# Optimization experiments

Hardware: AMD Instinct MI355X
Metric: run time of the kernel (lower is better)

The kernel has to match this reference:

```python
import jax, jax.numpy as jnp
import numpy as np

HIDDEN = 1280
NUM_HEADS = 16
NUM_KV_HEADS = 4
HEAD_DIM = 80
Q_SIZE = NUM_HEADS * HEAD_DIM          # 1280
KV_SIZE = NUM_KV_HEADS * HEAD_DIM      # 320
QKV_OUT = Q_SIZE + 2 * KV_SIZE         # 1920
R_SOFTPLUS_0 = 1.442695041


def setup_inputs() -> dict:
    key = jax.random.key(0)
    ks = jax.random.split(key, 6)
    B, S = 4, 2048
    return {
        "hidden_states": jax.random.normal(ks[0], (B, S, HIDDEN), dtype=jnp.float32),
        "scaling": jax.random.normal(ks[1], (HEAD_DIM,), dtype=jnp.float32),
        "qkv_w": jax.random.normal(ks[2], (QKV_OUT, HIDDEN), dtype=jnp.float32) * (1.0 / np.sqrt(HIDDEN)),
        "qkv_b": jax.random.normal(ks[3], (QKV_OUT,), dtype=jnp.float32) * 0.01,
        "o_w": jax.random.normal(ks[4], (HIDDEN, Q_SIZE), dtype=jnp.float32) * (1.0 / np.sqrt(Q_SIZE)),
        "o_b": jax.random.normal(ks[5], (HIDDEN,), dtype=jnp.float32) * 0.01,
    }


def reference(hidden_states, scaling, qkv_w, qkv_b, o_w, o_b):
    B, S, _ = hidden_states.shape
    qkv = hidden_states @ qkv_w.T + qkv_b                      # [B,S,1920]
    xq = qkv[..., :Q_SIZE].reshape(B, S, NUM_HEADS, HEAD_DIM)
    xk = qkv[..., Q_SIZE:Q_SIZE + KV_SIZE].reshape(B, S, NUM_KV_HEADS, HEAD_DIM)
    xv = qkv[..., Q_SIZE + KV_SIZE:].reshape(B, S, NUM_KV_HEADS, HEAD_DIM)
    # learned per-head-dim scaling: (r_softplus_0/sqrt(d)) * softplus(scaling)
    scale = (R_SOFTPLUS_0 / np.sqrt(HEAD_DIM)) * jax.nn.softplus(scaling)
    xq = xq * scale[None, None, None, :]
    # GQA: expand kv heads to match query heads (repeat_interleave on head dim)
    nq_per_kv = NUM_HEADS // NUM_KV_HEADS
    k = jnp.repeat(xk, nq_per_kv, axis=2)                      # [B,S,H,d]
    v = jnp.repeat(xv, nq_per_kv, axis=2)
    scores = jnp.einsum("bqhd,bkhd->bhqk", xq, k)              # [B,H,S,S]
    probs = jax.nn.softmax(scores.astype(jnp.float32), axis=-1).astype(xq.dtype)
    out = jnp.einsum("bhqk,bkhd->bqhd", probs, v)              # [B,S,H,d]
    out = out.reshape(B, S, Q_SIZE)
    return out @ o_w.T + o_b
```

## Files before the change

kernel.cpp:

```cpp
#include <hip/hip_runtime.h>

#define HIDDEN 1280
#define QOUT   1920
#define QSIZE  1280
#define KVSIZE 320
#define NHEAD  16
#define NKV    4
#define DH     80
#define SEQ    2048
#define BATCH  4
#define MTOT   (BATCH * SEQ)
#define NT64   (SEQ / 64)
#define KTILE_ELEMS 6144
#define VTILE_ELEMS 5760

typedef __attribute__((ext_vector_type(8))) short bf16x8;
typedef __attribute__((ext_vector_type(4))) float f32x4;

__device__ __forceinline__ unsigned short f2bf(float x) {
  union { float f; unsigned u; } v; v.f = x;
  unsigned r = v.u + 0x7fffu + ((v.u >> 16) & 1u);
  return (unsigned short)(r >> 16);
}

__device__ __forceinline__ unsigned packbf(float a, float b) {
  union { float f; unsigned u; } ua, ub;
  ua.f = a; ub.f = b;
  return __builtin_amdgcn_perm(ub.u + 0x8000u, ua.u + 0x8000u, 0x07060302u);
}

__device__ __forceinline__ float exp2x(float x) {
#if __has_builtin(__builtin_amdgcn_exp2f)
  return __builtin_amdgcn_exp2f(x);
#else
  return exp2f(x);
#endif
}

__device__ __forceinline__ void async_copy16(const void* g, void* lds) {
  __builtin_amdgcn_global_load_lds(
      (const __attribute__((address_space(1))) unsigned int*)g,
      (__attribute__((address_space(3))) unsigned int*)lds, 16, 0, 0);
}

#define HSB   (MTOT * HIDDEN / 4 / 256)
#define QWB   (QOUT * HIDDEN / 4 / 256)
#define OWB   (HIDDEN * QSIZE / 4 / 256)
__global__ __launch_bounds__(256) void prep_k(const float* __restrict__ hs,
                                              const float* __restrict__ qkv_w,
                                              const float* __restrict__ o_w,
                                              const float* __restrict__ scaling,
                                              unsigned short* __restrict__ hs_bf,
                                              unsigned short* __restrict__ qkvw_bf,
                                              unsigned short* __restrict__ ow_bf,
                                              float* __restrict__ cs) {
  const int bid = blockIdx.x, tid = threadIdx.x;
  const float* src; unsigned short* dst; int i;
  if (bid < HSB)            { src = hs;    dst = hs_bf;   i = bid * 256 + tid; }
  else if (bid < HSB + QWB) { src = qkv_w; dst = qkvw_bf; i = (bid - HSB) * 256 + tid; }
  else if (bid < HSB + QWB + OWB) { src = o_w; dst = ow_bf; i = (bid - HSB - QWB) * 256 + tid; }
  else {
    int n = (bid - HSB - QWB - OWB) * 256 + tid;
    if (n < QOUT) {
      float v = 1.0f;
      if (n < QSIZE) {
        float x = scaling[n % DH];
        float sp = (x > 20.f) ? x : log1pf(__expf(x));
        v = 1.442695041f * 1.442695041f * 0.11180339887f * sp;
      }
      cs[n] = v;
    }
    return;
  }
  float4 v = ((const float4*)src)[i];
  ushort4 o;
  o.x = f2bf(v.x); o.y = f2bf(v.y); o.z = f2bf(v.z); o.w = f2bf(v.w);
  ((ushort4*)dst)[i] = o;
}

template <bool OUT_BF16, bool USE_SCALE>
__global__ __launch_bounds__(256) void gemm_bt(const unsigned short* __restrict__ A,
                                               const unsigned short* __restrict__ Bt,
                                               const float* __restrict__ bias,
                                               const float* __restrict__ colscale,
                                               void* __restrict__ Cout,
                                               int M, int N, int K) {
  __shared__ unsigned short As[128 * 64];
  __shared__ unsigned short Bs[128 * 64];
  const int tid  = threadIdx.x;
  const int wave = tid >> 6, lane = tid & 63;
  const int r = lane & 15, quad = lane >> 4;
  const int xm = r & 7;
  const int m0 = blockIdx.y * 128, n0 = blockIdx.x * 128;
  const int rm = (wave >> 1) * 64, cn = (wave & 1) * 64;

  f32x4 acc[4][4];
#pragma unroll
  for (int i = 0; i < 4; ++i)
#pragma unroll
    for (int j = 0; j < 4; ++j) acc[i][j] = f32x4{0.f, 0.f, 0.f, 0.f};

  for (int k0 = 0; k0 < K; k0 += 64) {
    __syncthreads();
#pragma unroll
    for (int j = 0; j < 4; ++j) {
      const int c = tid + j * 256;
      const int row = c >> 3, sp = c & 7;
      const int sd = (sp ^ (row & 7)) * 8;
      async_copy16(A  + (size_t)(m0 + row) * K + k0 + sd, &As[c * 8]);
      async_copy16(Bt + (size_t)(n0 + row) * K + k0 + sd, &Bs[c * 8]);
    }
    __syncthreads();
#pragma unroll
    for (int kk = 0; kk < 2; ++kk) {
      bf16x8 af[4], bfr[4];
#pragma unroll
      for (int mi = 0; mi < 4; ++mi)
        af[mi] = *(const bf16x8*)&As[(rm + mi * 16 + r) * 64 + ((kk * 4 + quad) ^ xm) * 8];
#pragma unroll
      for (int ni = 0; ni < 4; ++ni)
        bfr[ni] = *(const bf16x8*)&Bs[(cn + ni * 16 + r) * 64 + ((kk * 4 + quad) ^ xm) * 8];
#pragma unroll
      for (int mi = 0; mi < 4; ++mi)
#pragma unroll
        for (int ni = 0; ni < 4; ++ni)
          acc[mi][ni] = __builtin_amdgcn_mfma_f32_16x16x32_bf16(af[mi], bfr[ni], acc[mi][ni], 0, 0, 0);
    }
  }

#pragma unroll
  for (int ni = 0; ni < 4; ++ni) {
    const int n = n0 + cn + ni * 16 + r;
    const float bn = bias[n];
    const float sc = USE_SCALE ? colscale[n] : 1.0f;
#pragma unroll
    for (int mi = 0; mi < 4; ++mi) {
#pragma unroll
      for (int reg = 0; reg < 4; ++reg) {
        const int m = m0 + rm + mi * 16 + quad * 4 + reg;
        const float v = (acc[mi][ni][reg] + bn) * sc;
        if (OUT_BF16)
          ((unsigned short*)Cout)[(size_t)m * N + n] = f2bf(v);
        else
          ((float*)Cout)[(size_t)m * N + n] = v;
      }
    }
  }
}

__global__ __launch_bounds__(256) void kvpack(const unsigned short* __restrict__ qkv,
                                              unsigned short* __restrict__ Kp,
                                              unsigned short* __restrict__ Vp) {
  const int st = blockIdx.x, kvh = blockIdx.y, b = blockIdx.z;
  const int tid = threadIdx.x;
  unsigned short* kout = Kp + (size_t)((b * NKV + kvh) * NT64 + st) * KTILE_ELEMS;
#pragma unroll
  for (int j = 0; j < 3; ++j) {
    int c = tid + j * 256;
    int row = c / 12, cir = c - row * 12;
    int kk = cir >> 2, sp = cir & 3;
    int sd = sp ^ ((row >> 1) & 3);
    int d0 = kk * 32 + sd * 8;
    uint4 v = {0, 0, 0, 0};
    if (d0 < DH)
      v = *(const uint4*)&qkv[(size_t)(b * SEQ + st * 64 + row) * QOUT +
                              QSIZE + kvh * DH + d0];
    *(uint4*)&kout[row * 96 + kk * 32 + sp * 8] = v;
  }
  __shared__ unsigned short tile[64][88];
  for (int c = tid; c < 640; c += 256) {
    int row = c / 10, seg = c % 10;
    uint4 v = *(const uint4*)&qkv[(size_t)(b * SEQ + st * 64 + row) * QOUT +
                                  QSIZE + KVSIZE + kvh * DH + seg * 8];
    *(uint4*)&tile[row][seg * 8] = v;
  }
  __syncthreads();
  unsigned short* vout = Vp + (size_t)((b * NKV + kvh) * NT64 + st) * VTILE_ELEMS;
  for (int c = tid; c < 5120; c += 256) {
    int d = c >> 6, key = c & 63;
    vout[d * 72 + key] = tile[key][d];
  }
}

__global__ __launch_bounds__(256, 2) void attn(const unsigned short* __restrict__ qkv,
                                               const unsigned short* __restrict__ Kp,
                                               const unsigned short* __restrict__ Vp,
                                               unsigned short* __restrict__ att) {
  const int qt = blockIdx.x, h = blockIdx.y, b = blockIdx.z;
  const int kvh = h >> 2;
  const int tid = threadIdx.x;
  const int wave = tid >> 6, lane = tid & 63;
  const int r = lane & 15, quad = lane >> 4;
  const int sq8 = (quad ^ ((r >> 1) & 3)) * 8;

  __shared__ unsigned short Ks[64 * 96];
  __shared__ unsigned short Vs[96 * 72];
  __shared__ unsigned short Ps[4][64 * 72];

  {
    const uint4 ones = {0x3F803F80u, 0x3F803F80u, 0x3F803F80u, 0x3F803F80u};
    for (int c = tid; c < 144; c += 256)
      *(uint4*)&Vs[80 * 72 + c * 8] = ones;
  }

  const int qbase = qt * 256 + wave * 64;
  bf16x8 qb[4][3];
#pragma unroll
  for (int t = 0; t < 4; ++t)
#pragma unroll
    for (int kk = 0; kk < 3; ++kk)
      qb[t][kk] = *(const bf16x8*)&qkv[(size_t)(b * SEQ + qbase + t * 16 + r) * QOUT +
                                       h * DH + kk * 32 + quad * 8];

  f32x4 o_acc[6][4];
#pragma unroll
  for (int i = 0; i < 6; ++i)
#pragma unroll
    for (int t = 0; t < 4; ++t) o_acc[i][t] = f32x4{0.f, 0.f, 0.f, 0.f};

  const unsigned short* kp = Kp + (size_t)((b * NKV + kvh) * NT64) * KTILE_ELEMS;
  const unsigned short* vp = Vp + (size_t)((b * NKV + kvh) * NT64) * VTILE_ELEMS;

  for (int kt = 0; kt < NT64; ++kt) {
    __syncthreads();
#pragma unroll
    for (int j = 0; j < 3; ++j)
      async_copy16(kp + (size_t)kt * KTILE_ELEMS + (tid + j * 256) * 8,
                   &Ks[(tid + j * 256) * 8]);
#pragma unroll
    for (int j = 0; j < 3; ++j) {
      int c = tid + j * 256;
      if (c < 720)
        async_copy16(vp + (size_t)kt * VTILE_ELEMS + c * 8, &Vs[c * 8]);
    }
    __syncthreads();

    f32x4 s[4][4];
#pragma unroll
    for (int nt = 0; nt < 4; ++nt) {
#pragma unroll
      for (int t = 0; t < 4; ++t) s[nt][t] = f32x4{0.f, 0.f, 0.f, 0.f};
#pragma unroll
      for (int kk = 0; kk < 3; ++kk) {
        bf16x8 ka = *(const bf16x8*)&Ks[(nt * 16 + r) * 96 + kk * 32 + sq8];
#pragma unroll
        for (int t = 0; t < 4; ++t)
          s[nt][t] = __builtin_amdgcn_mfma_f32_16x16x32_bf16(ka, qb[t][kk], s[nt][t], 0, 0, 0);
      }
    }

#pragma unroll
    for (int t = 0; t < 4; ++t)
#pragma unroll
      for (int nt = 0; nt < 4; ++nt) {
        uint2 w;
        w.x = packbf(exp2x(s[nt][t][0]), exp2x(s[nt][t][1]));
        w.y = packbf(exp2x(s[nt][t][2]), exp2x(s[nt][t][3]));
        *(uint2*)&Ps[wave][(t * 16 + r) * 72 + nt * 16 + quad * 4] = w;
      }
    __asm__ volatile("s_waitcnt lgkmcnt(0)" ::: "memory");

#pragma unroll
    for (int kh = 0; kh < 2; ++kh) {
      bf16x8 pb[4];
#pragma unroll
      for (int t = 0; t < 4; ++t)
        pb[t] = *(const bf16x8*)&Ps[wave][(t * 16 + r) * 72 + kh * 32 + quad * 8];
#pragma unroll
      for (int nt2 = 0; nt2 < 6; ++nt2) {
        bf16x8 va = *(const bf16x8*)&Vs[(nt2 * 16 + r) * 72 + kh * 32 + quad * 8];
#pragma unroll
        for (int t = 0; t < 4; ++t)
          o_acc[nt2][t] = __builtin_amdgcn_mfma_f32_16x16x32_bf16(va, pb[t], o_acc[nt2][t], 0, 0, 0);
      }
    }
  }

#pragma unroll
  for (int t = 0; t < 4; ++t) {
    const float il = 1.0f / o_acc[5][t][0];
    const size_t q = (size_t)(b * SEQ + qbase + t * 16 + r);
#pragma unroll
    for (int nt2 = 0; nt2 < 5; ++nt2) {
      uint2 w;
      w.x = packbf(o_acc[nt2][t][0] * il, o_acc[nt2][t][1] * il);
      w.y = packbf(o_acc[nt2][t][2] * il, o_acc[nt2][t][3] * il);
      *(uint2*)&att[q * QSIZE + h * DH + nt2 * 16 + quad * 4] = w;
    }
  }
}

extern "C" void kernel_launch(void* const* d_in, const int* in_sizes, int n_in,
                              void* d_out, int out_size, void* d_ws, size_t ws_size,
                              hipStream_t stream) {
  const float* hs      = (const float*)d_in[0];
  const float* scaling = (const float*)d_in[1];
  const float* qkv_w   = (const float*)d_in[2];
  const float* qkv_b   = (const float*)d_in[3];
  const float* o_w     = (const float*)d_in[4];
  const float* o_b     = (const float*)d_in[5];

  char* p = (char*)d_ws;
  unsigned short* hs_bf   = (unsigned short*)p; p += (size_t)MTOT * HIDDEN * 2;
  unsigned short* qkvw_bf = (unsigned short*)p; p += (size_t)QOUT * HIDDEN * 2;
  unsigned short* ow_bf   = (unsigned short*)p; p += (size_t)HIDDEN * QSIZE * 2;
  float* cscale           = (float*)p;          p += (size_t)QOUT * 4;
  unsigned short* qkv     = (unsigned short*)p; p += (size_t)MTOT * QOUT * 2;
  unsigned short* Kp      = (unsigned short*)p; p += (size_t)BATCH * NKV * NT64 * KTILE_ELEMS * 2;
  unsigned short* Vp      = (unsigned short*)p; p += (size_t)BATCH * NKV * NT64 * VTILE_ELEMS * 2;
  unsigned short* att     = hs_bf;

  prep_k<<<HSB + QWB + OWB + 8, 256, 0, stream>>>(hs, qkv_w, o_w, scaling,
                                                  hs_bf, qkvw_bf, ow_bf, cscale);

  dim3 g1(QOUT / 128, MTOT / 128);
  gemm_bt<true, true><<<g1, 256, 0, stream>>>(hs_bf, qkvw_bf, qkv_b, cscale, qkv,
                                              MTOT, QOUT, HIDDEN);
  dim3 gp(NT64, NKV, BATCH);
  kvpack<<<gp, 256, 0, stream>>>(qkv, Kp, Vp);
  dim3 g3(SEQ / 256, NHEAD, BATCH);
  attn<<<g3, 256, 0, stream>>>(qkv, Kp, Vp, att);
  dim3 g4(QSIZE / 128, MTOT / 128);
  gemm_bt<false, false><<<g4, 256, 0, stream>>>(att, ow_bf, o_b, nullptr, d_out,
                                                MTOT, QSIZE, HIDDEN);
}
```

Measured before the change: 322.0 us.

## Keep attention probabilities in registers and enlarge GEMM tiles to 256 rows

The attention kernel no longer writes exp'd scores to a per-wave LDS buffer and reads them back. It feeds the packed bf16 probabilities straight from the score accumulators into 16x16x16 MFMAs against V, one 16-key slice at a time. This removes LDS round-trips and a wait, and exp results are truncated rather than rounded to bf16. Separately, both projection GEMMs use 512-thread blocks covering 256 rows, which doubles A-tile reuse per B tile but raises LDS use and register pressure per block.

```diff
diff --git a/kernel.cpp b/kernel.cpp
--- a/kernel.cpp
+++ b/kernel.cpp
@@ -15,6 +15,7 @@
 #define VTILE_ELEMS 5760
 
 typedef __attribute__((ext_vector_type(8))) short bf16x8;
+typedef __attribute__((ext_vector_type(4))) short bf16x4;
 typedef __attribute__((ext_vector_type(4))) float f32x4;
 
 __device__ __forceinline__ unsigned short f2bf(float x) {
@@ -27,6 +28,12 @@
   union { float f; unsigned u; } ua, ub;
   ua.f = a; ub.f = b;
   return __builtin_amdgcn_perm(ub.u + 0x8000u, ua.u + 0x8000u, 0x07060302u);
+}
+
+__device__ __forceinline__ unsigned packbf_t(float a, float b) {
+  union { float f; unsigned u; } ua, ub;
+  ua.f = a; ub.f = b;
+  return __builtin_amdgcn_perm(ub.u, ua.u, 0x07060302u);
 }
 
 __device__ __forceinline__ float exp2x(float x) {
@@ -79,19 +86,19 @@
 }
 
 template <bool OUT_BF16, bool USE_SCALE>
-__global__ __launch_bounds__(256) void gemm_bt(const unsigned short* __restrict__ A,
+__global__ __launch_bounds__(512) void gemm_bt(const unsigned short* __restrict__ A,
                                                const unsigned short* __restrict__ Bt,
                                                const float* __restrict__ bias,
                                                const float* __restrict__ colscale,
                                                void* __restrict__ Cout,
                                                int M, int N, int K) {
-  __shared__ unsigned short As[128 * 64];
+  __shared__ unsigned short As[256 * 64];
   __shared__ unsigned short Bs[128 * 64];
   const int tid  = threadIdx.x;
   const int wave = tid >> 6, lane = tid & 63;
   const int r = lane & 15, quad = lane >> 4;
   const int xm = r & 7;
-  const int m0 = blockIdx.y * 128, n0 = blockIdx.x * 128;
+  const int m0 = blockIdx.y * 256, n0 = blockIdx.x * 128;
   const int rm = (wave >> 1) * 64, cn = (wave & 1) * 64;
 
   f32x4 acc[4][4];
@@ -104,10 +111,16 @@
     __syncthreads();
 #pragma unroll
     for (int j = 0; j < 4; ++j) {
-      const int c = tid + j * 256;
+      const int c = tid + j * 512;
       const int row = c >> 3, sp = c & 7;
       const int sd = (sp ^ (row & 7)) * 8;
-      async_copy16(A  + (size_t)(m0 + row) * K + k0 + sd, &As[c * 8]);
+      async_copy16(A + (size_t)(m0 + row) * K + k0 + sd, &As[c * 8]);
+    }
+#pragma unroll
+    for (int j = 0; j < 2; ++j) {
+      const int c = tid + j * 512;
+      const int row = c >> 3, sp = c & 7;
+      const int sd = (sp ^ (row & 7)) * 8;
       async_copy16(Bt + (size_t)(n0 + row) * K + k0 + sd, &Bs[c * 8]);
     }
     __syncthreads();
@@ -195,7 +208,6 @@
 
   __shared__ unsigned short Ks[64 * 96];
   __shared__ unsigned short Vs[96 * 72];
-  __shared__ unsigned short Ps[4][64 * 72];
 
   {
     const uint4 ones = {0x3F803F80u, 0x3F803F80u, 0x3F803F80u, 0x3F803F80u};
@@ -235,43 +247,38 @@
     }
     __syncthreads();
 
-    f32x4 s[4][4];
 #pragma unroll
     for (int nt = 0; nt < 4; ++nt) {
-#pragma unroll
-      for (int t = 0; t < 4; ++t) s[nt][t] = f32x4{0.f, 0.f, 0.f, 0.f};
-#pragma unroll
-      for (int kk = 0; kk < 3; ++kk) {
-        bf16x8 ka = *(const bf16x8*)&Ks[(nt * 16 + r) * 96 + kk * 32 + sq8];
+      bf16x8 ka[3];
+#pragma unroll
+      for (int kk = 0; kk < 3; ++kk)
+        ka[kk] = *(const bf16x8*)&Ks[(nt * 16 + r) * 96 + kk * 32 + sq8];
+
+      f32x4 s[4];
+#pragma unroll
+      for (int t = 0; t < 4; ++t) {
+        s[t] = f32x4{0.f, 0.f, 0.f, 0.f};
+#pragma unroll
+        for (int kk = 0; kk < 3; ++kk)
+          s[t] = __builtin_amdgcn_mfma_f32_16x16x32_bf16(ka[kk], qb[t][kk], s[t], 0, 0, 0);
+      }
+
+      bf16x4 pb[4];
+#pragma unroll
+      for (int t = 0; t < 4; ++t) {
+        union { uint2 u; bf16x4 v; } cv;
+        cv.u.x = packbf_t(exp2x(s[t][0]), exp2x(s[t][1]));
+        cv.u.y = packbf_t(exp2x(s[t][2]), exp2x(s[t][3]));
+        pb[t] = cv.v;
+      }
+
+#pragma unroll
+      for (int nt2 = 0; nt2 < 6; ++nt2) {
+        union { uint2 u; bf16x4 v; } va;
+        va.u = *(const uint2*)&Vs[(nt2 * 16 + r) * 72 + nt * 16 + quad * 4];
 #pragma unroll
         for (int t = 0; t < 4; ++t)
-          s[nt][t] = __builtin_amdgcn_mfma_f32_16x16x32_bf16(ka, qb[t][kk], s[nt][t], 0, 0, 0);
-      }
-    }
-
-#pragma unroll
-    for (int t = 0; t < 4; ++t)
-#pragma unroll
-      for (int nt = 0; nt < 4; ++nt) {
-        uint2 w;
-        w.x = packbf(exp2x(s[nt][t][0]), exp2x(s[nt][t][1]));
-        w.y = packbf(exp2x(s[nt][t][2]), exp2x(s[nt][t][3]));
-        *(uint2*)&Ps[wave][(t * 16 + r) * 72 + nt * 16 + quad * 4] = w;
-      }
-    __asm__ volatile("s_waitcnt lgkmcnt(0)" ::: "memory");
-
-#pragma unroll
-    for (int kh = 0; kh < 2; ++kh) {
-      bf16x8 pb[4];
-#pragma unroll
-      for (int t = 0; t < 4; ++t)
-        pb[t] = *(const bf16x8*)&Ps[wave][(t * 16 + r) * 72 + kh * 32 + quad * 8];
-#pragma unroll
-      for (int nt2 = 0; nt2 < 6; ++nt2) {
-        bf16x8 va = *(const bf16x8*)&Vs[(nt2 * 16 + r) * 72 + kh * 32 + quad * 8];
-#pragma unroll
-        for (int t = 0; t < 4; ++t)
-          o_acc[nt2][t] = __builtin_amdgcn_mfma_f32_16x16x32_bf16(va, pb[t], o_acc[nt2][t], 0, 0, 0);
+          o_acc[nt2][t] = __builtin_amdgcn_mfma_f32_16x16x16bf16_1k(va.v, pb[t], o_acc[nt2][t], 0, 0, 0);
       }
     }
   }
@@ -313,14 +320,14 @@
   prep_k<<<HSB + QWB + OWB + 8, 256, 0, stream>>>(hs, qkv_w, o_w, scaling,
                                                   hs_bf, qkvw_bf, ow_bf, cscale);
 
-  dim3 g1(QOUT / 128, MTOT / 128);
-  gemm_bt<true, true><<<g1, 256, 0, stream>>>(hs_bf, qkvw_bf, qkv_b, cscale, qkv,
+  dim3 g1(QOUT / 128, MTOT / 256);
+  gemm_bt<true, true><<<g1, 512, 0, stream>>>(hs_bf, qkvw_bf, qkv_b, cscale, qkv,
                                               MTOT, QOUT, HIDDEN);
   dim3 gp(NT64, NKV, BATCH);
   kvpack<<<gp, 256, 0, stream>>>(qkv, Kp, Vp);
   dim3 g3(SEQ / 256, NHEAD, BATCH);
   attn<<<g3, 256, 0, stream>>>(qkv, Kp, Vp, att);
-  dim3 g4(QSIZE / 128, MTOT / 128);
-  gemm_bt<false, false><<<g4, 256, 0, stream>>>(att, ow_bf, o_b, nullptr, d_out,
+  dim3 g4(QSIZE / 128, MTOT / 256);
+  gemm_bt<false, false><<<g4, 512, 0, stream>>>(att, ow_bf, o_b, nullptr, d_out,
                                                 MTOT, QSIZE, HIDDEN);
 }
```

Measured after the change: 300.1 us. 6.8% less time.
